# Optimization experiments

Hardware: AMD Instinct MI355X
Metric: run time of the kernel (lower is better)

## Reference

```python
import jax, jax.numpy as jnp
import numpy as np

N, E, G, D, H, C = 50000, 800000, 64, 128, 4, 32
EPS = 1e-5  # GraphNorm eps


def _gcn(x, W, b, src, dst, n):
    # PyG GCNConv: add self-loops (done by caller), symmetric norm D^-1/2 A D^-1/2
    xw = x @ W
    deg = jax.ops.segment_sum(jnp.ones_like(dst, dtype=xw.dtype), dst, num_segments=n)
    dinv = jnp.where(deg > 0, jax.lax.rsqrt(jnp.maximum(deg, 1e-12)), 0.0)
    norm = dinv[src] * dinv[dst]                      # [E2]
    out = jax.ops.segment_sum(xw[src] * norm[:, None], dst, num_segments=n)
    return out + b


def _gat(x, W, a_src, a_dst, b, src, dst, n):
    # PyG GATConv, heads=H, out C per head, concat, leaky_relu slope 0.2, self-loops added by caller
    h = (x @ W).reshape(n, H, C)
    es = jnp.einsum('nhc,hc->nh', h, a_src)
    ed = jnp.einsum('nhc,hc->nh', h, a_dst)
    e = jax.nn.leaky_relu(es[src] + ed[dst], 0.2)     # [E2,H]
    m = jax.ops.segment_max(e, dst, num_segments=n)   # per-dst softmax (stable)
    e = jnp.exp(e - m[dst])
    s = jax.ops.segment_sum(e, dst, num_segments=n)
    alpha = e / (s[dst] + 1e-16)
    out = jax.ops.segment_sum(h[src] * alpha[:, :, None], dst, num_segments=n)
    return out.reshape(n, H * C) + b


def _graphnorm(x, batch, w, b, ms, g):
    cnt = jnp.maximum(jax.ops.segment_sum(jnp.ones((x.shape[0],), x.dtype), batch, num_segments=g), 1.0)
    mean = jax.ops.segment_sum(x, batch, num_segments=g) / cnt[:, None]
    sub = x - ms * mean[batch]
    var = jax.ops.segment_sum(sub * sub, batch, num_segments=g) / cnt[:, None]
    return w * sub * jax.lax.rsqrt(var[batch] + EPS) + b


def setup_inputs() -> dict:
    key = jax.random.key(0)
    ks = jax.random.split(key, 40)

    def lin(k, din, dout):
        return jax.random.normal(k, (din, dout), jnp.float32) * np.float32((2.0 / (din + dout)) ** 0.5)

    inp = {
        'x': jax.random.normal(ks[0], (N, D), jnp.float32),
        'edge_index': jax.random.randint(ks[1], (2, E), 0, N, dtype=jnp.int32),
        'batch': jnp.sort(jax.random.randint(ks[2], (N,), 0, G, dtype=jnp.int32)),
        'Wp': lin(ks[3], D, D), 'bp': jnp.zeros((D,), jnp.float32),
        'Wg': lin(ks[4], D, D), 'bg': jnp.zeros((D,), jnp.float32),
        'Wa1': lin(ks[5], D, H * C), 'as1': jax.random.normal(ks[6], (H, C), jnp.float32) * 0.1,
        'ad1': jax.random.normal(ks[7], (H, C), jnp.float32) * 0.1, 'ba1': jnp.zeros((D,), jnp.float32),
        'Wa2': lin(ks[8], D, H * C), 'as2': jax.random.normal(ks[9], (H, C), jnp.float32) * 0.1,
        'ad2': jax.random.normal(ks[10], (H, C), jnp.float32) * 0.1, 'ba2': jnp.zeros((D,), jnp.float32),
        'gnw0': jnp.ones((D,), jnp.float32), 'gnb0': jnp.zeros((D,), jnp.float32), 'gns0': jnp.ones((D,), jnp.float32),
        'gnw1': jnp.ones((D,), jnp.float32), 'gnb1': jnp.zeros((D,), jnp.float32), 'gns1': jnp.ones((D,), jnp.float32),
        'gnw2': jnp.ones((D,), jnp.float32), 'gnb2': jnp.zeros((D,), jnp.float32), 'gns2': jnp.ones((D,), jnp.float32),
        'hw1': lin(ks[11], 2 * D, D), 'hb1': jnp.zeros((D,), jnp.float32),
        'hw2': lin(ks[12], D, D // 2), 'hb2': jnp.zeros((D // 2,), jnp.float32),
        'hw3': lin(ks[13], D // 2, 2), 'hb3': jnp.zeros((2,), jnp.float32),
        'nw1': lin(ks[14], D, D // 2), 'nb1': jnp.zeros((D // 2,), jnp.float32),
        'nw2': lin(ks[15], D // 2, 1), 'nb2': jnp.zeros((1,), jnp.float32),
    }
    return inp


def reference(x, edge_index, batch, Wp, bp, Wg, bg, Wa1, as1, ad1, ba1, Wa2, as2, ad2, ba2,
              gnw0, gnb0, gns0, gnw1, gnb1, gns1, gnw2, gnb2, gns2,
              hw1, hb1, hw2, hb2, hw3, hb3, nw1, nb1, nw2, nb2):
    n = x.shape[0]
    loop = jnp.arange(n, dtype=edge_index.dtype)
    src = jnp.concatenate([edge_index[0], loop])
    dst = jnp.concatenate([edge_index[1], loop])

    x = x @ Wp + bp
    h = _graphnorm(_gcn(x, Wg, bg, src, dst, n), batch, gnw0, gnb0, gns0, G)
    x = jax.nn.relu(h) + x  # dropout is identity in eval mode
    h = _graphnorm(_gat(x, Wa1, as1, ad1, ba1, src, dst, n), batch, gnw1, gnb1, gns1, G)
    x = jax.nn.relu(h) + x
    h = _graphnorm(_gat(x, Wa2, as2, ad2, ba2, src, dst, n), batch, gnw2, gnb2, gns2, G)
    x = jax.nn.relu(h) + x

    node_hub_scores = jax.nn.sigmoid((jax.nn.relu(x @ nw1 + nb1) @ nw2 + nb2)[:, 0])

    cnt = jnp.maximum(jax.ops.segment_sum(jnp.ones((n,), x.dtype), batch, num_segments=G), 1.0)
    gmean = jax.ops.segment_sum(x, batch, num_segments=G) / cnt[:, None]
    gmax = jax.ops.segment_max(x, batch, num_segments=G)
    graph_features = jnp.concatenate([gmean, gmax], axis=1)  # [G, 2D]

    z = jax.nn.relu(graph_features @ hw1 + hb1)
    z = jax.nn.relu(z @ hw2 + hb2)
    logits = z @ hw3 + hb3
    return (logits, node_hub_scores, graph_features, x)
```

## Files before the change

### kernel.cpp

```cpp
#include <hip/hip_runtime.h>
#include <cstdint>

#define D 128
#define GG 64
#define SLICES 16
#define NPASS 4

typedef short bf16x8 __attribute__((ext_vector_type(8)));
typedef float f32x4 __attribute__((ext_vector_type(4)));

__device__ inline unsigned short bf16u(float f) {
  unsigned u = __float_as_uint(f);
  u = (u + 0x7FFFu + ((u >> 16) & 1u)) >> 16;
  return (unsigned short)u;
}
__device__ inline float2 unpackbf2(unsigned u) {
  return make_float2(__uint_as_float(u << 16), __uint_as_float(u & 0xFFFF0000u));
}
__device__ inline void accum8(float* acc, uint4 v, float w) {
  float2 p0 = unpackbf2(v.x), p1 = unpackbf2(v.y), p2 = unpackbf2(v.z), p3 = unpackbf2(v.w);
  acc[0] += p0.x * w; acc[1] += p0.y * w; acc[2] += p1.x * w; acc[3] += p1.y * w;
  acc[4] += p2.x * w; acc[5] += p2.y * w; acc[6] += p3.x * w; acc[7] += p3.y * w;
}

__global__ void count_edges_k(const int* __restrict__ dst, int* __restrict__ cnt, int E) {
  int e = blockIdx.x * blockDim.x + threadIdx.x;
  if (e < E) atomicAdd(&cnt[dst[e]], 1);
}

__global__ void bounds_init_k(int* __restrict__ gstart, int* __restrict__ gend) {
  int g = threadIdx.x;
  gstart[g] = 0;
  gend[g] = 0;
}

__global__ void graph_bounds_k(const int* __restrict__ batch, int* __restrict__ gstart,
                               int* __restrict__ gend, int n) {
  int i = blockIdx.x * blockDim.x + threadIdx.x;
  if (i >= n) return;
  int b = batch[i];
  if (i == 0) {
    gstart[b] = 0;
  } else {
    int pb = batch[i - 1];
    if (pb != b) { gstart[b] = i; gend[pb] = i; }
  }
  if (i == n - 1) gend[b] = n;
}

__global__ void gcnt_k(const int* __restrict__ gstart, const int* __restrict__ gend,
                       int* __restrict__ gcnt) {
  int g = threadIdx.x;
  gcnt[g] = gend[g] - gstart[g];
}

__global__ __launch_bounds__(256) void scan1_k(const int* __restrict__ cnt, int* __restrict__ rp,
                                               int* __restrict__ bsum, int n) {
  __shared__ int sd[256];
  int t = threadIdx.x;
  int i = blockIdx.x * 256 + t;
  int v = (i < n) ? cnt[i] : 0;
  sd[t] = v;
  __syncthreads();
#pragma unroll
  for (int off = 1; off < 256; off <<= 1) {
    int u = (t >= off) ? sd[t - off] : 0;
    __syncthreads();
    sd[t] += u;
    __syncthreads();
  }
  if (i < n) rp[i] = sd[t] - v;
  if (t == 255) bsum[blockIdx.x] = sd[255];
}

__global__ __launch_bounds__(256) void scan2_k(int* __restrict__ bsum, int nb) {
  __shared__ int sd[256];
  int t = threadIdx.x;
  int v = (t < nb) ? bsum[t] : 0;
  sd[t] = v;
  __syncthreads();
#pragma unroll
  for (int off = 1; off < 256; off <<= 1) {
    int u = (t >= off) ? sd[t - off] : 0;
    __syncthreads();
    sd[t] += u;
    __syncthreads();
  }
  if (t < nb) bsum[t] = sd[t] - v;
}

__global__ __launch_bounds__(256) void scan3_k(int* __restrict__ rp, const int* __restrict__ bsum,
                                               int* __restrict__ cur, int n, int E) {
  int i = blockIdx.x * 256 + threadIdx.x;
  if (i < n) {
    int r = rp[i] + bsum[blockIdx.x];
    rp[i] = r;
    cur[i] = r;
  }
  if (i == 0) rp[n] = E;
}

__global__ __launch_bounds__(256) void fill_csr_mp_k(const int* __restrict__ src,
                                                     const int* __restrict__ dst,
                                                     int* __restrict__ cur, int* __restrict__ col,
                                                     int E, int slice, int chunks) {
  int pass = blockIdx.x / chunks;
  int e = (blockIdx.x % chunks) * 256 + threadIdx.x;
  if (e >= E) return;
  int d = dst[e];
  if (d >= pass * slice && d < (pass + 1) * slice) {
    int p = atomicAdd(&cur[d], 1);
    col[p] = src[e];
  }
}

__global__ void dinv_k(const int* __restrict__ cnt, float* __restrict__ dinv, int n) {
  int i = blockIdx.x * blockDim.x + threadIdx.x;
  if (i < n) dinv[i] = rsqrtf((float)cnt[i] + 1.0f);
}

__global__ void cast_bf16_k(const float* __restrict__ in, unsigned short* __restrict__ outp, int n4) {
  int i = blockIdx.x * blockDim.x + threadIdx.x;
  if (i >= n4) return;
  float4 v = ((const float4*)in)[i];
  ushort4 o;
  o.x = bf16u(v.x); o.y = bf16u(v.y); o.z = bf16u(v.z); o.w = bf16u(v.w);
  ((ushort4*)outp)[i] = o;
}

__global__ void packB_k(const float* __restrict__ B, unsigned short* __restrict__ Bp, int ldb, int ct) {
  int idx = blockIdx.x * 256 + threadIdx.x;
  if (idx >= ct * 256) return;
  int lane = idx & 63;
  int kc = (idx >> 6) & 3;
  int c = idx >> 8;
  int kb = kc * 32 + (lane >> 4) * 8;
  int colq = c * 16 + (lane & 15);
  unsigned short o[8];
#pragma unroll
  for (int j = 0; j < 8; ++j) o[j] = bf16u(B[(size_t)(kb + j) * ldb + colq]);
  uint4 p;
  p.x = (unsigned)o[0] | ((unsigned)o[1] << 16);
  p.y = (unsigned)o[2] | ((unsigned)o[3] << 16);
  p.z = (unsigned)o[4] | ((unsigned)o[5] << 16);
  p.w = (unsigned)o[6] | ((unsigned)o[7] << 16);
  *(uint4*)&Bp[(size_t)idx * 8] = p;
}

__global__ __launch_bounds__(256) void gemm_mfma_k(const unsigned short* __restrict__ Ab,
                                                   const unsigned short* __restrict__ Bp,
                                                   const float* __restrict__ bias,
                                                   float* __restrict__ Cf,
                                                   unsigned short* __restrict__ Cb, int M) {
  __shared__ unsigned short Bs[16384];
  int t = threadIdx.x;
  for (int i = t; i < 2048; i += 256) ((uint4*)Bs)[i] = ((const uint4*)Bp)[i];
  __syncthreads();
  int w = t >> 6, lane = t & 63;
  int row0 = blockIdx.x * 64 + w * 16;
  int arow = row0 + (lane & 15);
  f32x4 acc[8];
#pragma unroll
  for (int c = 0; c < 8; ++c) acc[c] = {0.f, 0.f, 0.f, 0.f};
#pragma unroll
  for (int kc = 0; kc < 4; ++kc) {
    bf16x8 a = {0, 0, 0, 0, 0, 0, 0, 0};
    if (arow < M) a = *(const bf16x8*)&Ab[(size_t)arow * 128 + kc * 32 + (lane >> 4) * 8];
#pragma unroll
    for (int c = 0; c < 8; ++c) {
      bf16x8 b = *(const bf16x8*)&Bs[((c * 4 + kc) * 64 + lane) * 8];
      acc[c] = __builtin_amdgcn_mfma_f32_16x16x32_bf16(a, b, acc[c], 0, 0, 0);
    }
  }
  int rbase = row0 + (lane >> 4) * 4;
#pragma unroll
  for (int c = 0; c < 8; ++c) {
    int colq = c * 16 + (lane & 15);
    float bb = bias ? bias[colq] : 0.f;
#pragma unroll
    for (int r = 0; r < 4; ++r) {
      int row = rbase + r;
      if (row < M) {
        float v = acc[c][r] + bb;
        if (Cf) Cf[(size_t)row * 128 + colq] = v;
        if (Cb) Cb[(size_t)row * 128 + colq] = bf16u(v);
      }
    }
  }
}

__global__ __launch_bounds__(256) void gcn_gather_k(const uint4* __restrict__ xw16,
                                                    const int* __restrict__ rp, const int* __restrict__ col,
                                                    const float* __restrict__ dinv, const float* __restrict__ bias,
                                                    float* __restrict__ out, int n) {
  int i = blockIdx.x * 4 + (threadIdx.x >> 6);
  if (i >= n) return;
  int lane = threadIdx.x & 63;
  int g = lane >> 4, sub = lane & 15;
  int e0 = __builtin_amdgcn_readfirstlane(rp[i]);
  int e1 = __builtin_amdgcn_readfirstlane(rp[i + 1]);
  float di = dinv[i];
  float acc[8] = {0.f, 0.f, 0.f, 0.f, 0.f, 0.f, 0.f, 0.f};
  if (g == 0) {
    uint4 v = xw16[(size_t)i * 16 + sub];
    accum8(acc, v, di * di);
  }
  int e = e0;
  for (; e + 15 < e1; e += 16) {
    int s0 = col[e + g];
    int s1 = col[e + 4 + g];
    int s2 = col[e + 8 + g];
    int s3 = col[e + 12 + g];
    float w0 = dinv[s0] * di, w1 = dinv[s1] * di, w2 = dinv[s2] * di, w3 = dinv[s3] * di;
    uint4 v0 = xw16[(size_t)s0 * 16 + sub];
    uint4 v1 = xw16[(size_t)s1 * 16 + sub];
    uint4 v2 = xw16[(size_t)s2 * 16 + sub];
    uint4 v3 = xw16[(size_t)s3 * 16 + sub];
    accum8(acc, v0, w0); accum8(acc, v1, w1); accum8(acc, v2, w2); accum8(acc, v3, w3);
  }
  for (; e < e1; e += 4) {
    bool ok = (e + g) < e1;
    int s0 = ok ? col[e + g] : i;
    float w0 = ok ? dinv[s0] * di : 0.f;
    uint4 v0 = xw16[(size_t)s0 * 16 + sub];
    accum8(acc, v0, w0);
  }
#pragma unroll
  for (int k = 0; k < 8; ++k) {
    acc[k] += __shfl_xor(acc[k], 16, 64);
    acc[k] += __shfl_xor(acc[k], 32, 64);
  }
  if (g == 0) {
    float4 b0 = ((const float4*)bias)[sub * 2], b1 = ((const float4*)bias)[sub * 2 + 1];
    *(float4*)&out[(size_t)i * 128 + sub * 8] =
        make_float4(acc[0] + b0.x, acc[1] + b0.y, acc[2] + b0.z, acc[3] + b0.w);
    *(float4*)&out[(size_t)i * 128 + sub * 8 + 4] =
        make_float4(acc[4] + b1.x, acc[5] + b1.y, acc[6] + b1.z, acc[7] + b1.w);
  }
}

__global__ void attn_coef_k(const unsigned short* __restrict__ hb, const float* __restrict__ a_s,
                            const float* __restrict__ a_d, float* __restrict__ es,
                            float* __restrict__ ed, int n) {
  int idx = blockIdx.x * blockDim.x + threadIdx.x;
  if (idx >= n * 4) return;
  int node = idx >> 2, hh = idx & 3;
  const uint4* hr = (const uint4*)(hb + (size_t)node * 128 + hh * 32);
  const float4* av = (const float4*)(a_s + hh * 32);
  const float4* dv = (const float4*)(a_d + hh * 32);
  float s = 0.f, d2 = 0.f;
#pragma unroll
  for (int q = 0; q < 4; ++q) {
    uint4 u = hr[q];
    float2 p0 = unpackbf2(u.x), p1 = unpackbf2(u.y), p2 = unpackbf2(u.z), p3 = unpackbf2(u.w);
    float4 a0 = av[q * 2], a1 = av[q * 2 + 1];
    float4 d0 = dv[q * 2], d1 = dv[q * 2 + 1];
    s  += p0.x * a0.x + p0.y * a0.y + p1.x * a0.z + p1.y * a0.w
        + p2.x * a1.x + p2.y * a1.y + p3.x * a1.z + p3.y * a1.w;
    d2 += p0.x * d0.x + p0.y * d0.y + p1.x * d0.z + p1.y * d0.w
        + p2.x * d1.x + p2.y * d1.y + p3.x * d1.z + p3.y * d1.w;
  }
  es[idx] = s;
  ed[idx] = d2;
}

__global__ __launch_bounds__(256) void alpha_k(const float* __restrict__ es, const float* __restrict__ ed,
                                               const int* __restrict__ rp, const int* __restrict__ col,
                                               float* __restrict__ alpha, float* __restrict__ aself,
                                               float* __restrict__ winv, int n) {
  int i = blockIdx.x * 4 + (threadIdx.x >> 6);
  if (i >= n) return;
  int lane = threadIdx.x & 63;
  int hh = lane >> 4, slot = lane & 15;
  int e0 = __builtin_amdgcn_readfirstlane(rp[i]);
  int e1 = __builtin_amdgcn_readfirstlane(rp[i + 1]);
  float edi = ed[i * 4 + hh];
  float esf = es[i * 4 + hh] + edi;
  esf = esf >= 0.f ? esf : 0.2f * esf;
  float m = esf;
  for (int e = e0 + slot; e < e1; e += 16) {
    int sj = col[e];
    float ev = es[sj * 4 + hh] + edi;
    ev = ev >= 0.f ? ev : 0.2f * ev;
    alpha[(size_t)e * 4 + hh] = ev;
    m = fmaxf(m, ev);
  }
#pragma unroll
  for (int off = 1; off < 16; off <<= 1) m = fmaxf(m, __shfl_xor(m, off, 64));
  float s = (slot == 0) ? __expf(esf - m) : 0.f;
  for (int e = e0 + slot; e < e1; e += 16) {
    float w = __expf(alpha[(size_t)e * 4 + hh] - m);
    alpha[(size_t)e * 4 + hh] = w;
    s += w;
  }
#pragma unroll
  for (int off = 1; off < 16; off <<= 1) s += __shfl_xor(s, off, 64);
  if (slot == 0) {
    aself[i * 4 + hh] = __expf(esf - m);
    winv[i * 4 + hh] = 1.0f / (s + 1e-16f);
  }
}

__global__ __launch_bounds__(256) void gat_gather_k(const uint4* __restrict__ hf16,
                                                    const int* __restrict__ rp, const int* __restrict__ col,
                                                    const float* __restrict__ alpha, const float* __restrict__ aself,
                                                    const float* __restrict__ winv,
                                                    const float* __restrict__ bias, float* __restrict__ out, int n) {
  int i = blockIdx.x * 4 + (threadIdx.x >> 6);
  if (i >= n) return;
  int lane = threadIdx.x & 63;
  int g = lane >> 4, sub = lane & 15;
  int hh = sub >> 2;
  int e0 = __builtin_amdgcn_readfirstlane(rp[i]);
  int e1 = __builtin_amdgcn_readfirstlane(rp[i + 1]);
  float acc[8] = {0.f, 0.f, 0.f, 0.f, 0.f, 0.f, 0.f, 0.f};
  if (g == 0) {
    uint4 v = hf16[(size_t)i * 16 + sub];
    accum8(acc, v, aself[i * 4 + hh]);
  }
  int e = e0;
  for (; e + 15 < e1; e += 16) {
    int s0 = col[e + g];
    int s1 = col[e + 4 + g];
    int s2 = col[e + 8 + g];
    int s3 = col[e + 12 + g];
    float a0 = alpha[(size_t)(e + g) * 4 + hh];
    float a1 = alpha[(size_t)(e + 4 + g) * 4 + hh];
    float a2 = alpha[(size_t)(e + 8 + g) * 4 + hh];
    float a3 = alpha[(size_t)(e + 12 + g) * 4 + hh];
    uint4 v0 = hf16[(size_t)s0 * 16 + sub];
    uint4 v1 = hf16[(size_t)s1 * 16 + sub];
    uint4 v2 = hf16[(size_t)s2 * 16 + sub];
    uint4 v3 = hf16[(size_t)s3 * 16 + sub];
    accum8(acc, v0, a0); accum8(acc, v1, a1); accum8(acc, v2, a2); accum8(acc, v3, a3);
  }
  for (; e < e1; e += 4) {
    bool ok = (e + g) < e1;
    int s0 = ok ? col[e + g] : i;
    float a0 = ok ? alpha[(size_t)(e + g) * 4 + hh] : 0.f;
    uint4 v0 = hf16[(size_t)s0 * 16 + sub];
    accum8(acc, v0, a0);
  }
#pragma unroll
  for (int k = 0; k < 8; ++k) {
    acc[k] += __shfl_xor(acc[k], 16, 64);
    acc[k] += __shfl_xor(acc[k], 32, 64);
  }
  if (g == 0) {
    float wi = winv[i * 4 + hh];
    float4 b0 = ((const float4*)bias)[sub * 2], b1 = ((const float4*)bias)[sub * 2 + 1];
    *(float4*)&out[(size_t)i * 128 + sub * 8] =
        make_float4(acc[0] * wi + b0.x, acc[1] * wi + b0.y, acc[2] * wi + b0.z, acc[3] * wi + b0.w);
    *(float4*)&out[(size_t)i * 128 + sub * 8 + 4] =
        make_float4(acc[4] * wi + b1.x, acc[5] * wi + b1.y, acc[6] * wi + b1.z, acc[7] * wi + b1.w);
  }
}

__global__ __launch_bounds__(256) void gn_stats_k(const float* __restrict__ h, const int* __restrict__ gstart,
                                                  const int* __restrict__ gcnt, float* __restrict__ gsum,
                                                  float* __restrict__ gsq) {
  int g = blockIdx.x / SLICES, sl = blockIdx.x % SLICES;
  int st = gstart[g], cn = gcnt[g];
  int d = threadIdx.x & 127, half = threadIdx.x >> 7;
  float s = 0.f, ss = 0.f;
  for (int r = sl * 2 + half; r < cn; r += 2 * SLICES) {
    float v = h[(size_t)(st + r) * D + d];
    s += v; ss += v * v;
  }
  __shared__ float l1[128], l2[128];
  if (half) { l1[d] = s; l2[d] = ss; }
  __syncthreads();
  if (!half) {
    atomicAdd(&gsum[g * D + d], s + l1[d]);
    atomicAdd(&gsq[g * D + d], ss + l2[d]);
  }
}

__global__ void gn_finalize_k(const float* __restrict__ gsum, const float* __restrict__ gsq,
                              const int* __restrict__ gcnt, const float* __restrict__ ms,
                              float* __restrict__ mean, float* __restrict__ rstd) {
  int g = blockIdx.x, d = threadIdx.x;
  float cnt = fmaxf((float)gcnt[g], 1.0f);
  float mu = gsum[g * D + d] / cnt;
  float m2 = gsq[g * D + d] / cnt;
  float s = ms[d];
  float var = m2 - (2.0f * s - s * s) * mu * mu;
  mean[g * D + d] = mu;
  rstd[g * D + d] = rsqrtf(fmaxf(var, 0.0f) + 1e-5f);
}

__global__ void gn_apply_k(const float* __restrict__ h, float* __restrict__ x,
                           unsigned short* __restrict__ xb,
                           const int* __restrict__ batch, const float* __restrict__ mean,
                           const float* __restrict__ rstd, const float* __restrict__ w,
                           const float* __restrict__ b, const float* __restrict__ ms, int n) {
  int idx = blockIdx.x * blockDim.x + threadIdx.x;
  if (idx >= n * 32) return;
  int node = idx >> 5, q = idx & 31;
  int g = batch[node];
  int d0 = q * 4;
  float4 hv = ((const float4*)h)[idx];
  float4 xv = ((const float4*)x)[idx];
  float ha[4] = {hv.x, hv.y, hv.z, hv.w};
  float xa[4] = {xv.x, xv.y, xv.z, xv.w};
  float ra[4];
#pragma unroll
  for (int j = 0; j < 4; ++j) {
    int d = d0 + j;
    float sub = ha[j] - ms[d] * mean[g * D + d];
    float v = w[d] * sub * rstd[g * D + d] + b[d];
    ra[j] = fmaxf(v, 0.f) + xa[j];
  }
  ((float4*)x)[idx] = make_float4(ra[0], ra[1], ra[2], ra[3]);
  ushort4 o;
  o.x = bf16u(ra[0]); o.y = bf16u(ra[1]); o.z = bf16u(ra[2]); o.w = bf16u(ra[3]);
  ((ushort4*)xb)[idx] = o;
}

__global__ __launch_bounds__(256) void hub_mfma_k(const unsigned short* __restrict__ Xb,
                                                  const unsigned short* __restrict__ W1p,
                                                  const float* __restrict__ nb1, const float* __restrict__ nw2,
                                                  const float* __restrict__ nb2, float* __restrict__ out, int n) {
  __shared__ unsigned short Bs[8192];
  int t = threadIdx.x;
  for (int i = t; i < 1024; i += 256) ((uint4*)Bs)[i] = ((const uint4*)W1p)[i];
  __syncthreads();
  int w = t >> 6, lane = t & 63;
  int row0 = blockIdx.x * 64 + w * 16;
  int arow = row0 + (lane & 15);
  f32x4 acc[4];
#pragma unroll
  for (int c = 0; c < 4; ++c) acc[c] = {0.f, 0.f, 0.f, 0.f};
#pragma unroll
  for (int kc = 0; kc < 4; ++kc) {
    bf16x8 a = {0, 0, 0, 0, 0, 0, 0, 0};
    if (arow < n) a = *(const bf16x8*)&Xb[(size_t)arow * 128 + kc * 32 + (lane >> 4) * 8];
#pragma unroll
    for (int c = 0; c < 4; ++c) {
      bf16x8 b = *(const bf16x8*)&Bs[((c * 4 + kc) * 64 + lane) * 8];
      acc[c] = __builtin_amdgcn_mfma_f32_16x16x32_bf16(a, b, acc[c], 0, 0, 0);
    }
  }
  float b2 = nb2[0];
  float s[4] = {0.f, 0.f, 0.f, 0.f};
#pragma unroll
  for (int c = 0; c < 4; ++c) {
    int colq = c * 16 + (lane & 15);
    float b1 = nb1[colq];
    float w2 = nw2[colq];
#pragma unroll
    for (int r = 0; r < 4; ++r) s[r] += fmaxf(acc[c][r] + b1, 0.f) * w2;
  }
#pragma unroll
  for (int off = 1; off < 16; off <<= 1) {
#pragma unroll
    for (int r = 0; r < 4; ++r) s[r] += __shfl_xor(s[r], off, 64);
  }
  if ((lane & 15) == 0) {
    int rbase = row0 + (lane >> 4) * 4;
#pragma unroll
    for (int r = 0; r < 4; ++r) {
      int row = rbase + r;
      if (row < n) out[row] = 1.0f / (1.0f + __expf(-(s[r] + b2)));
    }
  }
}

__global__ void init_maxu_k(unsigned* __restrict__ p, int n) {
  int i = blockIdx.x * blockDim.x + threadIdx.x;
  if (i < n) p[i] = 0x007FFFFFu;
}

__global__ __launch_bounds__(256) void pool_stats_k(const float* __restrict__ x, const int* __restrict__ gstart,
                                                    const int* __restrict__ gcnt, float* __restrict__ gsum,
                                                    unsigned* __restrict__ gmaxu) {
  int g = blockIdx.x / SLICES, sl = blockIdx.x % SLICES;
  int st = gstart[g], cn = gcnt[g];
  int d = threadIdx.x & 127, half = threadIdx.x >> 7;
  float s = 0.f, mx = __uint_as_float(0xFF800000u);
  for (int r = sl * 2 + half; r < cn; r += 2 * SLICES) {
    float v = x[(size_t)(st + r) * D + d];
    s += v; mx = fmaxf(mx, v);
  }
  __shared__ float l1[128], l2[128];
  if (half) { l1[d] = s; l2[d] = mx; }
  __syncthreads();
  if (!half) {
    s += l1[d];
    mx = fmaxf(mx, l2[d]);
    atomicAdd(&gsum[g * D + d], s);
    unsigned u = __float_as_uint(mx);
    u = (u & 0x80000000u) ? ~u : (u | 0x80000000u);
    atomicMax(&gmaxu[g * D + d], u);
  }
}

__global__ void pool_fin_k(const float* __restrict__ gsum, const unsigned* __restrict__ gmaxu,
                           const int* __restrict__ gcnt, float* __restrict__ gf) {
  int g = blockIdx.x, d = threadIdx.x;
  float cnt = fmaxf((float)gcnt[g], 1.0f);
  gf[g * 256 + d] = gsum[g * D + d] / cnt;
  unsigned u = gmaxu[g * D + d];
  unsigned bits = (u & 0x80000000u) ? (u ^ 0x80000000u) : ~u;
  gf[g * 256 + 128 + d] = __uint_as_float(bits);
}

__global__ __launch_bounds__(128) void mlp_k(const float* __restrict__ gf, const float* __restrict__ hw1,
                                             const float* __restrict__ hb1, const float* __restrict__ hw2,
                                             const float* __restrict__ hb2, const float* __restrict__ hw3,
                                             const float* __restrict__ hb3, float* __restrict__ logits) {
  __shared__ float sg[256], z1[128], z2[64];
  int g = blockIdx.x, t = threadIdx.x;
  sg[t] = gf[g * 256 + t];
  sg[t + 128] = gf[g * 256 + 128 + t];
  __syncthreads();
  float a = hb1[t];
  for (int k = 0; k < 256; ++k) a += sg[k] * hw1[k * 128 + t];
  z1[t] = fmaxf(a, 0.f);
  __syncthreads();
  if (t < 64) {
    float a2 = hb2[t];
    for (int k = 0; k < 128; ++k) a2 += z1[k] * hw2[k * 64 + t];
    z2[t] = fmaxf(a2, 0.f);
  }
  __syncthreads();
  if (t < 2) {
    float a3 = hb3[t];
    for (int k = 0; k < 64; ++k) a3 += z2[k] * hw3[k * 2 + t];
    logits[g * 2 + t] = a3;
  }
}

extern "C" void kernel_launch(void* const* d_in, const int* in_sizes, int n_in,
                              void* d_out, int out_size, void* d_ws, size_t ws_size,
                              hipStream_t stream) {
  const float* x_in  = (const float*)d_in[0];
  const int*   eidx  = (const int*)d_in[1];
  const int*   batch = (const int*)d_in[2];
  const float* Wp  = (const float*)d_in[3];
  const float* bp  = (const float*)d_in[4];
  const float* Wg  = (const float*)d_in[5];
  const float* bg  = (const float*)d_in[6];
  const float* Wa1 = (const float*)d_in[7];
  const float* as1 = (const float*)d_in[8];
  const float* ad1 = (const float*)d_in[9];
  const float* ba1 = (const float*)d_in[10];
  const float* Wa2 = (const float*)d_in[11];
  const float* as2 = (const float*)d_in[12];
  const float* ad2 = (const float*)d_in[13];
  const float* ba2 = (const float*)d_in[14];
  const float* gnw[3] = {(const float*)d_in[15], (const float*)d_in[18], (const float*)d_in[21]};
  const float* gnb[3] = {(const float*)d_in[16], (const float*)d_in[19], (const float*)d_in[22]};
  const float* gns[3] = {(const float*)d_in[17], (const float*)d_in[20], (const float*)d_in[23]};
  const float* hw1 = (const float*)d_in[24];
  const float* hb1 = (const float*)d_in[25];
  const float* hw2 = (const float*)d_in[26];
  const float* hb2 = (const float*)d_in[27];
  const float* hw3 = (const float*)d_in[28];
  const float* hb3 = (const float*)d_in[29];
  const float* nw1 = (const float*)d_in[30];
  const float* nb1 = (const float*)d_in[31];
  const float* nw2 = (const float*)d_in[32];
  const float* nb2 = (const float*)d_in[33];

  const int N = in_sizes[0] / D;
  const int E = in_sizes[1] / 2;
  const int* src = eidx;
  const int* dst = eidx + E;

  float* out    = (float*)d_out;
  float* logits = out;
  float* hub    = out + GG * 2;
  float* gf     = out + GG * 2 + N;
  float* X      = out + GG * 2 + N + GG * 256;

  char* wp = (char*)d_ws;
  auto alloc = [&](size_t bytes) { char* p = wp; wp += (bytes + 255) & ~(size_t)255; return p; };
  float*    B1    = (float*)alloc((size_t)N * D * 4);
  float*    B2    = (float*)alloc((size_t)N * D * 4);
  unsigned* B1h   = (unsigned*)alloc((size_t)N * (D / 2) * 4);
  unsigned short* Xb = (unsigned short*)alloc((size_t)N * D * 2);
  int*   col     = (int*)alloc((size_t)E * 4);
  int*   cnt     = (int*)alloc((size_t)N * 4);
  int*   rowp    = (int*)alloc((size_t)(N + 1) * 4);
  int*   cur     = (int*)alloc((size_t)N * 4);
  float* dinv    = (float*)alloc((size_t)N * 4);
  float* es      = (float*)alloc((size_t)N * 4 * 4);
  float* ed      = (float*)alloc((size_t)N * 4 * 4);
  float* aself   = (float*)alloc((size_t)N * 4 * 4);
  float* winv    = (float*)alloc((size_t)N * 4 * 4);
  float* gsum    = (float*)alloc((size_t)GG * D * 4);
  float* gsq     = (float*)alloc((size_t)GG * D * 4);
  unsigned* gmaxu = (unsigned*)alloc((size_t)GG * D * 4);
  float* mean    = (float*)alloc((size_t)GG * D * 4);
  float* rstd    = (float*)alloc((size_t)GG * D * 4);
  int*   gcnt    = (int*)alloc((size_t)GG * 4);
  int*   gstart  = (int*)alloc((size_t)GG * 4);
  int*   gend    = (int*)alloc((size_t)GG * 4);
  int*   bsum    = (int*)alloc((size_t)256 * 4);
  unsigned short* Wpp  = (unsigned short*)alloc(16384 * 2);
  unsigned short* Wgp  = (unsigned short*)alloc(16384 * 2);
  unsigned short* Wa1p = (unsigned short*)alloc(16384 * 2);
  unsigned short* Wa2p = (unsigned short*)alloc(16384 * 2);
  unsigned short* W1p  = (unsigned short*)alloc(8192 * 2);
  float* alpha = B1;
  unsigned short* xinb = (unsigned short*)B2;
  if ((size_t)(wp - (char*)d_ws) > ws_size) return;

  const int nb = (N + 255) / 256;

  hipMemsetAsync(cnt, 0, (size_t)N * 4, stream);
  count_edges_k<<<(E + 255) / 256, 256, 0, stream>>>(dst, cnt, E);
  bounds_init_k<<<1, GG, 0, stream>>>(gstart, gend);
  graph_bounds_k<<<nb, 256, 0, stream>>>(batch, gstart, gend, N);
  gcnt_k<<<1, GG, 0, stream>>>(gstart, gend, gcnt);
  scan1_k<<<nb, 256, 0, stream>>>(cnt, rowp, bsum, N);
  scan2_k<<<1, 256, 0, stream>>>(bsum, nb);
  scan3_k<<<nb, 256, 0, stream>>>(rowp, bsum, cur, N, E);
  dinv_k<<<nb, 256, 0, stream>>>(cnt, dinv, N);
  {
    int chunks = (E + 255) / 256;
    int slice = (N + NPASS - 1) / NPASS;
    fill_csr_mp_k<<<chunks * NPASS, 256, 0, stream>>>(src, dst, cur, col, E, slice, chunks);
  }

  packB_k<<<8, 256, 0, stream>>>(Wp, Wpp, 128, 8);
  packB_k<<<8, 256, 0, stream>>>(Wg, Wgp, 128, 8);
  packB_k<<<8, 256, 0, stream>>>(Wa1, Wa1p, 128, 8);
  packB_k<<<8, 256, 0, stream>>>(Wa2, Wa2p, 128, 8);
  packB_k<<<4, 256, 0, stream>>>(nw1, W1p, 64, 4);
  cast_bf16_k<<<(N * 32 + 255) / 256, 256, 0, stream>>>(x_in, xinb, N * 32);

  const int gemmGrid = (N + 63) / 64;
  const int aggGrid  = (N + 3) / 4;

  auto graphnorm = [&](int layer) {
    hipMemsetAsync(gsum, 0, 2 * (size_t)GG * D * 4, stream);
    gn_stats_k<<<GG * SLICES, 256, 0, stream>>>(B2, gstart, gcnt, gsum, gsq);
    gn_finalize_k<<<GG, D, 0, stream>>>(gsum, gsq, gcnt, gns[layer], mean, rstd);
    gn_apply_k<<<(N * 32 + 255) / 256, 256, 0, stream>>>(B2, X, Xb, batch, mean, rstd,
                                                         gnw[layer], gnb[layer], gns[layer], N);
  };

  gemm_mfma_k<<<gemmGrid, 256, 0, stream>>>(xinb, Wpp, bp, X, Xb, N);

  gemm_mfma_k<<<gemmGrid, 256, 0, stream>>>(Xb, Wgp, nullptr, nullptr, (unsigned short*)B1h, N);
  gcn_gather_k<<<aggGrid, 256, 0, stream>>>((const uint4*)B1h, rowp, col, dinv, bg, B2, N);
  graphnorm(0);

  gemm_mfma_k<<<gemmGrid, 256, 0, stream>>>(Xb, Wa1p, nullptr, nullptr, (unsigned short*)B1h, N);
  attn_coef_k<<<(N * 4 + 255) / 256, 256, 0, stream>>>((const unsigned short*)B1h, as1, ad1, es, ed, N);
  alpha_k<<<aggGrid, 256, 0, stream>>>(es, ed, rowp, col, alpha, aself, winv, N);
  gat_gather_k<<<aggGrid, 256, 0, stream>>>((const uint4*)B1h, rowp, col, alpha, aself, winv, ba1, B2, N);
  graphnorm(1);

  gemm_mfma_k<<<gemmGrid, 256, 0, stream>>>(Xb, Wa2p, nullptr, nullptr, (unsigned short*)B1h, N);
  attn_coef_k<<<(N * 4 + 255) / 256, 256, 0, stream>>>((const unsigned short*)B1h, as2, ad2, es, ed, N);
  alpha_k<<<aggGrid, 256, 0, stream>>>(es, ed, rowp, col, alpha, aself, winv, N);
  gat_gather_k<<<aggGrid, 256, 0, stream>>>((const uint4*)B1h, rowp, col, alpha, aself, winv, ba2, B2, N);
  graphnorm(2);

  hub_mfma_k<<<gemmGrid, 256, 0, stream>>>(Xb, W1p, nb1, nw2, nb2, hub, N);

  hipMemsetAsync(gsum, 0, (size_t)GG * D * 4, stream);
  init_maxu_k<<<(GG * D + 255) / 256, 256, 0, stream>>>(gmaxu, GG * D);
  pool_stats_k<<<GG * SLICES, 256, 0, stream>>>(X, gstart, gcnt, gsum, gmaxu);
  pool_fin_k<<<GG, D, 0, stream>>>(gsum, gmaxu, gcnt, gf);
  mlp_k<<<GG, 128, 0, stream>>>(gf, hw1, hb1, hw2, hb2, hw3, hb3, logits);
}
```

Before: 458.2 us.

## Store CSR column indices as 16-bit and split CSR fill across XCDs

Measured after the change: 454.1 us. No clear change (-0.9%).

```diff
diff --git a/kernel.cpp b/kernel.cpp
--- a/kernel.cpp
+++ b/kernel.cpp
@@ -4,7 +4,7 @@
 #define D 128
 #define GG 64
 #define SLICES 16
-#define NPASS 4
+#define NXCD 8
 
 typedef short bf16x8 __attribute__((ext_vector_type(8)));
 typedef float f32x4 __attribute__((ext_vector_type(4)));
@@ -90,33 +90,31 @@
 }
 
 __global__ __launch_bounds__(256) void scan3_k(int* __restrict__ rp, const int* __restrict__ bsum,
-                                               int* __restrict__ cur, int n, int E) {
+                                               int* __restrict__ cur, const int* __restrict__ cnt,
+                                               float* __restrict__ dinv, int n, int E) {
   int i = blockIdx.x * 256 + threadIdx.x;
   if (i < n) {
     int r = rp[i] + bsum[blockIdx.x];
     rp[i] = r;
     cur[i] = r;
+    dinv[i] = rsqrtf((float)cnt[i] + 1.0f);
   }
   if (i == 0) rp[n] = E;
 }
 
-__global__ __launch_bounds__(256) void fill_csr_mp_k(const int* __restrict__ src,
-                                                     const int* __restrict__ dst,
-                                                     int* __restrict__ cur, int* __restrict__ col,
-                                                     int E, int slice, int chunks) {
-  int pass = blockIdx.x / chunks;
-  int e = (blockIdx.x % chunks) * 256 + threadIdx.x;
+__global__ __launch_bounds__(256) void fill_csr_xcd_k(const int* __restrict__ src,
+                                                      const int* __restrict__ dst,
+                                                      int* __restrict__ cur,
+                                                      unsigned short* __restrict__ col,
+                                                      int E, int slice) {
+  int pass = blockIdx.x & (NXCD - 1);
+  int e = (blockIdx.x >> 3) * 256 + threadIdx.x;
   if (e >= E) return;
   int d = dst[e];
-  if (d >= pass * slice && d < (pass + 1) * slice) {
+  if ((unsigned)(d - pass * slice) < (unsigned)slice) {
     int p = atomicAdd(&cur[d], 1);
-    col[p] = src[e];
-  }
-}
-
-__global__ void dinv_k(const int* __restrict__ cnt, float* __restrict__ dinv, int n) {
-  int i = blockIdx.x * blockDim.x + threadIdx.x;
-  if (i < n) dinv[i] = rsqrtf((float)cnt[i] + 1.0f);
+    col[p] = (unsigned short)src[e];
+  }
 }
 
 __global__ void cast_bf16_k(const float* __restrict__ in, unsigned short* __restrict__ outp, int n4) {
@@ -190,7 +188,8 @@
 }
 
 __global__ __launch_bounds__(256) void gcn_gather_k(const uint4* __restrict__ xw16,
-                                                    const int* __restrict__ rp, const int* __restrict__ col,
+                                                    const int* __restrict__ rp,
+                                                    const unsigned short* __restrict__ col,
                                                     const float* __restrict__ dinv, const float* __restrict__ bias,
                                                     float* __restrict__ out, int n) {
   int i = blockIdx.x * 4 + (threadIdx.x >> 6);
@@ -220,7 +219,7 @@
   }
   for (; e < e1; e += 4) {
     bool ok = (e + g) < e1;
-    int s0 = ok ? col[e + g] : i;
+    int s0 = ok ? (int)col[e + g] : i;
     float w0 = ok ? dinv[s0] * di : 0.f;
     uint4 v0 = xw16[(size_t)s0 * 16 + sub];
     accum8(acc, v0, w0);
@@ -265,7 +264,8 @@
 }
 
 __global__ __launch_bounds__(256) void alpha_k(const float* __restrict__ es, const float* __restrict__ ed,
-                                               const int* __restrict__ rp, const int* __restrict__ col,
+                                               const int* __restrict__ rp,
+                                               const unsigned short* __restrict__ col,
                                                float* __restrict__ alpha, float* __restrict__ aself,
                                                float* __restrict__ winv, int n) {
   int i = blockIdx.x * 4 + (threadIdx.x >> 6);
@@ -302,7 +302,8 @@
 }
 
 __global__ __launch_bounds__(256) void gat_gather_k(const uint4* __restrict__ hf16,
-                                                    const int* __restrict__ rp, const int* __restrict__ col,
+                                                    const int* __restrict__ rp,
+                                                    const unsigned short* __restrict__ col,
                                                     const float* __restrict__ alpha, const float* __restrict__ aself,
                                                     const float* __restrict__ winv,
                                                     const float* __restrict__ bias, float* __restrict__ out, int n) {
@@ -336,7 +337,7 @@
   }
   for (; e < e1; e += 4) {
     bool ok = (e + g) < e1;
-    int s0 = ok ? col[e + g] : i;
+    int s0 = ok ? (int)col[e + g] : i;
     float a0 = ok ? alpha[(size_t)(e + g) * 4 + hh] : 0.f;
     uint4 v0 = hf16[(size_t)s0 * 16 + sub];
     accum8(acc, v0, a0);
@@ -580,7 +581,7 @@
   float*    B2    = (float*)alloc((size_t)N * D * 4);
   unsigned* B1h   = (unsigned*)alloc((size_t)N * (D / 2) * 4);
   unsigned short* Xb = (unsigned short*)alloc((size_t)N * D * 2);
-  int*   col     = (int*)alloc((size_t)E * 4);
+  unsigned short* col = (unsigned short*)alloc((size_t)E * 2);
   int*   cnt     = (int*)alloc((size_t)N * 4);
   int*   rowp    = (int*)alloc((size_t)(N + 1) * 4);
   int*   cur     = (int*)alloc((size_t)N * 4);
@@ -616,12 +617,11 @@
   gcnt_k<<<1, GG, 0, stream>>>(gstart, gend, gcnt);
   scan1_k<<<nb, 256, 0, stream>>>(cnt, rowp, bsum, N);
   scan2_k<<<1, 256, 0, stream>>>(bsum, nb);
-  scan3_k<<<nb, 256, 0, stream>>>(rowp, bsum, cur, N, E);
-  dinv_k<<<nb, 256, 0, stream>>>(cnt, dinv, N);
+  scan3_k<<<nb, 256, 0, stream>>>(rowp, bsum, cur, cnt, dinv, N, E);
   {
     int chunks = (E + 255) / 256;
-    int slice = (N + NPASS - 1) / NPASS;
-    fill_csr_mp_k<<<chunks * NPASS, 256, 0, stream>>>(src, dst, cur, col, E, slice, chunks);
+    int slice = (N + NXCD - 1) / NXCD;
+    fill_csr_xcd_k<<<chunks * NXCD, 256, 0, stream>>>(src, dst, cur, col, E, slice);
   }
 
   packB_k<<<8, 256, 0, stream>>>(Wp, Wpp, 128, 8);
```
